# Kernel tuning notes

Hardware: AMD Instinct MI355X
Metric: run time of the kernel (lower is better)

Reference implementation:

```python
import jax, jax.numpy as jnp
import numpy as np

D_MODEL = 1024
NUM_HEADS = 16
THETA = 10000.0
B, T = 2, 2048


def _rope(x, pos, theta_base):
    # x: (b, h, t, d_h); interleaved pairs (x0,x1),(x2,x3),... per the
    # rearrange '... (c d) -> ... c d' with d=2 in the original module.
    d = x.shape[-1]
    half = d // 2
    inv_freq = 1.0 / (theta_base ** (2.0 * jnp.arange(half, dtype=jnp.float32) / d))
    ang = pos.astype(jnp.float32)[:, None] * inv_freq[None, :]  # (t, half)
    sin = jnp.sin(ang)[None, None]  # (1,1,t,half)
    cos = jnp.cos(ang)[None, None]
    x1 = x[..., 0::2]
    x2 = x[..., 1::2]
    r1 = x1 * cos - x2 * sin
    r2 = x1 * sin + x2 * cos
    return jnp.stack([r1, r2], axis=-1).reshape(x.shape)


def setup_inputs() -> dict:
    key = jax.random.key(0)
    k0, k1, k2, k3, k4 = jax.random.split(key, 5)
    sigma = (2.0 / (D_MODEL + D_MODEL)) ** 0.5
    return {
        "in_features": jax.random.normal(k0, (B, T, D_MODEL), dtype=jnp.float32),
        "Wq": jax.random.normal(k1, (D_MODEL, D_MODEL), dtype=jnp.float32) * sigma,
        "Wk": jax.random.normal(k2, (D_MODEL, D_MODEL), dtype=jnp.float32) * sigma,
        "Wv": jax.random.normal(k3, (D_MODEL, D_MODEL), dtype=jnp.float32) * sigma,
        "Wo": jax.random.normal(k4, (D_MODEL, D_MODEL), dtype=jnp.float32) * sigma,
        "token_positions": jnp.arange(T, dtype=jnp.int32),
    }


def reference(in_features, Wq, Wk, Wv, Wo, token_positions):
    b, t, d_model = in_features.shape
    h = NUM_HEADS
    d_h = d_model // h
    # Fused-style QKV projections (x @ W.T, weights stored (in, out))
    q = in_features @ Wq.T
    k = in_features @ Wk.T
    v = in_features @ Wv.T
    # (b, t, h*d_h) -> (b, h, t, d_h)
    q = q.reshape(b, t, h, d_h).transpose(0, 2, 1, 3)
    k = k.reshape(b, t, h, d_h).transpose(0, 2, 1, 3)
    v = v.reshape(b, t, h, d_h).transpose(0, 2, 1, 3)
    q = _rope(q, token_positions, THETA)
    k = _rope(k, token_positions, THETA)
    scale = 1.0 / jnp.sqrt(jnp.asarray(d_h, dtype=q.dtype))
    scores = jnp.einsum('bhqd,bhkd->bhqk', q, k) * scale
    causal = jnp.tril(jnp.ones((t, t), dtype=bool))
    scores = jnp.where(causal[None, None], scores, -jnp.inf)
    attn = jax.nn.softmax(scores, axis=-1)
    out = jnp.einsum('bhqk,bhkd->bhqd', attn, v)
    out = out.transpose(0, 2, 1, 3).reshape(b, t, h * d_h)
    return out @ Wo.T
```

## Files before the change

kernel.cpp:

```cpp
#include <hip/hip_runtime.h>

#define D_MODEL 1024
#define NUM_HEADS 16
#define DH 64
#define B_SZ 2
#define T_SZ 2048
#define M_ROWS (B_SZ * T_SZ)

typedef __bf16 bf16;
typedef __bf16 bf16x4 __attribute__((ext_vector_type(4)));
typedef __bf16 bf16x8 __attribute__((ext_vector_type(8)));
typedef float f32x4 __attribute__((ext_vector_type(4)));

__device__ __forceinline__ void async_copy16(const bf16* g, bf16* l) {
  __builtin_amdgcn_global_load_lds(
      (const __attribute__((address_space(1))) void*)g,
      (__attribute__((address_space(3))) void*)l, 16, 0, 0);
}

#define NX (M_ROWS * D_MODEL / 4)
#define NW (D_MODEL * D_MODEL / 4)

__global__ __launch_bounds__(256) void cast_all(
    const float* __restrict__ X, const float* __restrict__ Wq,
    const float* __restrict__ Wk, const float* __restrict__ Wv,
    const float* __restrict__ Wo,
    bf16* __restrict__ Xb, bf16* __restrict__ Wqb, bf16* __restrict__ Wkb,
    bf16* __restrict__ Wvb, bf16* __restrict__ Wob) {
  int i = blockIdx.x * 256 + threadIdx.x;
  const float* s; bf16* d; int off;
  if (i < NX) {
    s = X; d = Xb; off = i;
  } else {
    int j = i - NX;
    int w = j >> 18;
    off = j & (NW - 1);
    if (w == 0)      { s = Wq; d = Wqb; }
    else if (w == 1) { s = Wk; d = Wkb; }
    else if (w == 2) { s = Wv; d = Wvb; }
    else             { s = Wo; d = Wob; }
  }
  float4 v = ((const float4*)s)[off];
  bf16x4 o;
  o[0] = (bf16)v.x; o[1] = (bf16)v.y; o[2] = (bf16)v.z; o[3] = (bf16)v.w;
  ((bf16x4*)d)[off] = o;
}

#define KLN 0.28782313662425f
#define BK 32
#define NKT (D_MODEL / BK)

__global__ __launch_bounds__(512, 4) void qkv_gemm(
    const bf16* __restrict__ Xb,
    const bf16* __restrict__ Wqb, const bf16* __restrict__ Wkb,
    const bf16* __restrict__ Wvb, const int* __restrict__ pos,
    bf16* __restrict__ Q, bf16* __restrict__ K, bf16* __restrict__ VT) {
  __shared__ bf16 LA[3][128 * BK];
  __shared__ bf16 LB[3][256 * BK];

  int tid = threadIdx.x;
  int wave = tid >> 6, lane = tid & 63;
  int wm = wave >> 2, wn = wave & 3;
  int l15 = lane & 15, quad = lane >> 4;

  int row0 = blockIdx.x * 128;
  int col0 = blockIdx.y * 256;
  int sel = col0 >> 10;
  int nb = col0 & 1023;
  const bf16* W = (sel == 0) ? Wqb : (sel == 1) ? Wkb : Wvb;

  int srow = tid >> 2;
  int scol = 8 * ((tid & 3) ^ ((tid >> 3) & 3));
  const bf16* Ag = Xb + (size_t)(row0 + srow) * D_MODEL + scol;
  const bf16* Bg = W + (size_t)(nb + srow) * D_MODEL + scol;
  int ldst = tid * 8;

  int swz = 8 * (quad ^ ((l15 >> 1) & 3));
  int aoff = (wm * 64 + l15) * BK + swz;
  int boff = (wn * 64 + l15) * BK + swz;

  f32x4 acc[4][4];
#pragma unroll
  for (int mi = 0; mi < 4; ++mi)
#pragma unroll
    for (int nj = 0; nj < 4; ++nj) acc[mi][nj] = (f32x4){0.f, 0.f, 0.f, 0.f};

#define STAGE(bq, pt)                                                        \
  do {                                                                       \
    int k0_ = (pt) * BK;                                                     \
    async_copy16(Ag + k0_, &LA[bq][ldst]);                                   \
    async_copy16(Bg + k0_, &LB[bq][ldst]);                                   \
    async_copy16(Bg + k0_ + (size_t)128 * D_MODEL, &LB[bq][ldst + 4096]);    \
  } while (0)

  STAGE(0, 0);
  STAGE(1, 1);
  asm volatile("s_waitcnt vmcnt(3)" ::: "memory");
  __builtin_amdgcn_s_barrier();
  __builtin_amdgcn_sched_barrier(0);

  int cur = 0;
  for (int kt = 0; kt < NKT; ++kt) {
    const bf16* La = LA[cur];
    const bf16* Lb = LB[cur];
    bf16x8 a[4], b[4];
#pragma unroll
    for (int mi = 0; mi < 4; ++mi)
      a[mi] = *(const bf16x8*)&La[aoff + mi * 16 * BK];
#pragma unroll
    for (int nj = 0; nj < 4; ++nj)
      b[nj] = *(const bf16x8*)&Lb[boff + nj * 16 * BK];

    if (kt + 2 < NKT) {
      int nbuf = cur + 2 >= 3 ? cur - 1 : cur + 2;
      STAGE(nbuf, kt + 2);
      asm volatile("s_waitcnt vmcnt(3) lgkmcnt(0)" ::: "memory");
    } else {
      asm volatile("s_waitcnt vmcnt(0) lgkmcnt(0)" ::: "memory");
    }
    __builtin_amdgcn_s_barrier();
    __builtin_amdgcn_sched_barrier(0);

    __builtin_amdgcn_s_setprio(1);
#pragma unroll
    for (int mi = 0; mi < 4; ++mi)
#pragma unroll
      for (int nj = 0; nj < 4; ++nj)
        acc[mi][nj] = __builtin_amdgcn_mfma_f32_16x16x32_bf16(
            a[mi], b[nj], acc[mi][nj], 0, 0, 0);
    __builtin_amdgcn_s_setprio(0);

    cur = cur == 2 ? 0 : cur + 1;
  }
#undef STAGE

  if (sel == 1) {
    bool even = (l15 & 1) == 0;
#pragma unroll
    for (int nj = 0; nj < 4; ++nj) {
      float fr = __expf(-(float)((nj * 16 + (l15 & 14)) >> 1) * KLN);
#pragma unroll
      for (int mi = 0; mi < 4; ++mi)
#pragma unroll
        for (int r = 0; r < 4; ++r) {
          float p = (float)pos[(row0 + wm * 64 + mi * 16 + quad * 4 + r) &
                               (T_SZ - 1)];
          float v = acc[mi][nj][r];
          float pn = __shfl_xor(v, 1);
          float s, c;
          __sincosf(p * fr, &s, &c);
          acc[mi][nj][r] = even ? (v * c - pn * s) : (pn * s + v * c);
        }
    }
  }

  if (sel == 2) {
    int b = row0 >> 11;
    int t0 = row0 & (T_SZ - 1);
#pragma unroll
    for (int mi = 0; mi < 4; ++mi) {
      int t = t0 + wm * 64 + mi * 16 + quad * 4;
#pragma unroll
      for (int nj = 0; nj < 4; ++nj) {
        int col = nb + wn * 64 + nj * 16 + l15;
        int h = col >> 6;
        int d = col & 63;
        bf16x4 ov;
#pragma unroll
        for (int r = 0; r < 4; ++r) ov[r] = (bf16)acc[mi][nj][r];
        *(bf16x4*)&VT[((size_t)(b * NUM_HEADS + h) * DH + d) * T_SZ + t] = ov;
      }
    }
  } else {
    bf16* Out = (sel == 0) ? Q : K;
#pragma unroll
    for (int mi = 0; mi < 4; ++mi) {
      int row = row0 + wm * 64 + mi * 16 + quad * 4;
#pragma unroll
      for (int nj = 0; nj < 4; ++nj) {
        int col = nb + wn * 64 + nj * 16 + l15;
#pragma unroll
        for (int r = 0; r < 4; ++r)
          Out[(size_t)(row + r) * D_MODEL + col] = (bf16)acc[mi][nj][r];
      }
    }
  }
}

#define KST 72

__global__ __launch_bounds__(256, 3) void attn_kernel(
    const bf16* __restrict__ Q, const bf16* __restrict__ K,
    const bf16* __restrict__ VT, const int* __restrict__ pos,
    bf16* __restrict__ AO) {
  __shared__ bf16 KV[2 * 64 * KST];
  __shared__ float lred[4][4][16];
  bf16* Kt = KV;
  bf16* Vt = KV + 64 * KST;

  int bh = blockIdx.x;
  int qi = 31 - (int)blockIdx.y;
  int bb = bh >> 4, h = bh & 15;
  int tid = threadIdx.x;
  int wave = tid >> 6, lane = tid & 63;
  int l15 = lane & 15, quad = lane >> 4;
  int w16 = wave * 16;

  int q0 = qi * 64;
  size_t grow = (size_t)bb * T_SZ + q0;

  bf16x8 bq[4][2];
#pragma unroll
  for (int qt = 0; qt < 4; ++qt) {
    const bf16* Qp = Q + (grow + qt * 16 + l15) * D_MODEL + h * DH + quad * 8;
    bq[qt][0] = *(const bf16x8*)(Qp);
    bq[qt][1] = *(const bf16x8*)(Qp + 32);
    float p = (float)pos[q0 + qt * 16 + l15];
#pragma unroll
    for (int jj = 0; jj < 4; ++jj) {
      int i0 = quad * 4 + jj;
      float s, c;
      __sincosf(p * __expf(-(float)i0 * KLN), &s, &c);
      float x1 = (float)bq[qt][0][2 * jj], x2 = (float)bq[qt][0][2 * jj + 1];
      bq[qt][0][2 * jj]     = (bf16)(x1 * c - x2 * s);
      bq[qt][0][2 * jj + 1] = (bf16)(x1 * s + x2 * c);
      __sincosf(p * __expf(-(float)(i0 + 16) * KLN), &s, &c);
      float y1 = (float)bq[qt][1][2 * jj], y2 = (float)bq[qt][1][2 * jj + 1];
      bq[qt][1][2 * jj]     = (bf16)(y1 * c - y2 * s);
      bq[qt][1][2 * jj + 1] = (bf16)(y1 * s + y2 * c);
    }
  }

  f32x4 o[4][4];
#pragma unroll
  for (int dt = 0; dt < 4; ++dt)
#pragma unroll
    for (int qt = 0; qt < 4; ++qt) o[dt][qt] = (f32x4){0.f, 0.f, 0.f, 0.f};
  float l_acc[4] = {0.f, 0.f, 0.f, 0.f};

  int srow = tid >> 2;
  int sc = (tid & 3) * 16;
  const bf16* Kg = K + ((size_t)bb * T_SZ + srow) * D_MODEL + h * DH + sc;
  const bf16* Vg = VT + ((size_t)bh * DH + srow) * T_SZ + sc;
  bf16* Kl = &Kt[srow * KST + sc];
  bf16* Vl = &Vt[srow * KST + sc];

  int nchunks = qi + 1;

  bf16x8 kr0 = *(const bf16x8*)(Kg);
  bf16x8 kr1 = *(const bf16x8*)(Kg + 8);
  bf16x8 vr0 = *(const bf16x8*)(Vg);
  bf16x8 vr1 = *(const bf16x8*)(Vg + 8);

  for (int t = 0; t < nchunks; ++t) {
    __syncthreads();
    *(bf16x8*)(Kl) = kr0;
    *(bf16x8*)(Kl + 8) = kr1;
    *(bf16x8*)(Vl) = vr0;
    *(bf16x8*)(Vl + 8) = vr1;
    if (t + 1 < nchunks) {
      const bf16* Kn = Kg + (size_t)(t + 1) * 64 * D_MODEL;
      const bf16* Vn = Vg + (t + 1) * 64;
      kr0 = *(const bf16x8*)(Kn);
      kr1 = *(const bf16x8*)(Kn + 8);
      vr0 = *(const bf16x8*)(Vn);
      vr1 = *(const bf16x8*)(Vn + 8);
    }
    __syncthreads();

    bf16x8 ak0 = *(const bf16x8*)&Kt[(w16 + l15) * KST + quad * 8];
    bf16x8 ak1 = *(const bf16x8*)&Kt[(w16 + l15) * KST + 32 + quad * 8];
    f32x4 st[4];
#pragma unroll
    for (int qt = 0; qt < 4; ++qt) {
      f32x4 s4 = (f32x4){0.f, 0.f, 0.f, 0.f};
      s4 = __builtin_amdgcn_mfma_f32_16x16x32_bf16(ak0, bq[qt][0], s4, 0, 0, 0);
      s4 = __builtin_amdgcn_mfma_f32_16x16x32_bf16(ak1, bq[qt][1], s4, 0, 0, 0);
      st[qt] = s4;
    }

    bool last = (t == nchunks - 1);
    bf16x4 pb[4];
#pragma unroll
    for (int qt = 0; qt < 4; ++qt) {
      float ps = 0.f;
#pragma unroll
      for (int j = 0; j < 4; ++j) {
        float p = __expf(st[qt][j] * 0.125f);
        if (last) {
          int cl = w16 + quad * 4 + j;
          p = (cl > qt * 16 + l15) ? 0.f : p;
        }
        pb[qt][j] = (bf16)p;
        ps += p;
      }
      l_acc[qt] += ps;
    }

#pragma unroll
    for (int dt = 0; dt < 4; ++dt) {
      bf16x4 vb = *(const bf16x4*)&Vt[(dt * 16 + l15) * KST + w16 + quad * 4];
#pragma unroll
      for (int qt = 0; qt < 4; ++qt)
        asm("v_mfma_f32_16x16x16_bf16 %0, %1, %2, %0"
            : "+v"(o[dt][qt])
            : "v"(pb[qt]), "v"(vb));
    }
  }

#pragma unroll
  for (int qt = 0; qt < 4; ++qt) {
    l_acc[qt] += __shfl_xor(l_acc[qt], 16);
    l_acc[qt] += __shfl_xor(l_acc[qt], 32);
  }
  if (lane < 16) {
#pragma unroll
    for (int qt = 0; qt < 4; ++qt) lred[wave][qt][lane] = l_acc[qt];
  }

  __syncthreads();
  float* red = (float*)KV;

#pragma unroll
  for (int s = 1; s <= 3; ++s) {
#pragma unroll
    for (int qt = 0; qt < 4; ++qt)
      if (((qt - s) & 3) == wave) {
#pragma unroll
        for (int dt = 0; dt < 4; ++dt)
          *(f32x4*)&red[qt * 1024 + dt * 256 + lane * 4] = o[dt][qt];
      }
    __syncthreads();
#pragma unroll
    for (int qt = 0; qt < 4; ++qt)
      if (qt == wave) {
#pragma unroll
        for (int dt = 0; dt < 4; ++dt)
          o[dt][qt] += *(const f32x4*)&red[qt * 1024 + dt * 256 + lane * 4];
      }
    __syncthreads();
  }

#pragma unroll
  for (int qt = 0; qt < 4; ++qt)
    if (qt == wave) {
      float inv[4];
#pragma unroll
      for (int r = 0; r < 4; ++r) {
        int qq = quad * 4 + r;
        float ls = lred[0][qt][qq] + lred[1][qt][qq] + lred[2][qt][qq] +
                   lred[3][qt][qq];
        inv[r] = 1.0f / ls;
      }
#pragma unroll
      for (int dt = 0; dt < 4; ++dt)
#pragma unroll
        for (int r = 0; r < 4; ++r)
          AO[(grow + qt * 16 + quad * 4 + r) * D_MODEL + h * DH + dt * 16 +
             l15] = (bf16)(o[dt][qt][r] * inv[r]);
    }
}

__global__ __launch_bounds__(256) void out_gemm(
    const bf16* __restrict__ AO, const bf16* __restrict__ Wob,
    float* __restrict__ out) {
  __shared__ bf16 As[128 * 32];
  __shared__ bf16 Bs[64 * 32];

  int tid = threadIdx.x;
  int wave = tid >> 6, lane = tid & 63;
  int l15 = lane & 15, quad = lane >> 4;

  int row0 = blockIdx.x * 128;
  int nb = blockIdx.y * 64;

  int srow = tid >> 2;
  int schunk = tid & 3;
  const bf16* Ag = AO + (size_t)(row0 + srow) * D_MODEL + schunk * 8;
  const bf16* Bg = Wob + (size_t)(nb + srow) * D_MODEL + schunk * 8;
  bf16* Al0 = &As[srow * 32 + schunk * 8];
  bf16* Al1 = &As[(srow + 64) * 32 + schunk * 8];
  bf16* Bl = &Bs[srow * 32 + schunk * 8];

  f32x4 acc[2][4];
#pragma unroll
  for (int i = 0; i < 2; ++i)
#pragma unroll
    for (int j = 0; j < 4; ++j) acc[i][j] = (f32x4){0.f, 0.f, 0.f, 0.f};

  for (int k0 = 0; k0 < D_MODEL; k0 += 32) {
    async_copy16(Ag + k0, Al0);
    async_copy16(Ag + k0 + (size_t)64 * D_MODEL, Al1);
    async_copy16(Bg + k0, Bl);
    __syncthreads();

    bf16x8 af[2], bfr[4];
#pragma unroll
    for (int i = 0; i < 2; ++i)
      af[i] = *(const bf16x8*)&As[(wave * 32 + i * 16 + l15) * 32 + quad * 8];
#pragma unroll
    for (int j = 0; j < 4; ++j)
      bfr[j] = *(const bf16x8*)&Bs[(j * 16 + l15) * 32 + quad * 8];
#pragma unroll
    for (int i = 0; i < 2; ++i)
#pragma unroll
      for (int j = 0; j < 4; ++j)
        acc[i][j] = __builtin_amdgcn_mfma_f32_16x16x32_bf16(af[i], bfr[j],
                                                            acc[i][j], 0, 0, 0);
    __syncthreads();
  }

#pragma unroll
  for (int i = 0; i < 2; ++i) {
    int row = row0 + wave * 32 + i * 16 + quad * 4;
#pragma unroll
    for (int j = 0; j < 4; ++j) {
      int col = nb + j * 16 + l15;
#pragma unroll
      for (int r = 0; r < 4; ++r)
        out[(size_t)(row + r) * D_MODEL + col] = acc[i][j][r];
    }
  }
}

extern "C" void kernel_launch(void* const* d_in, const int* in_sizes, int n_in,
                              void* d_out, int out_size, void* d_ws, size_t ws_size,
                              hipStream_t stream) {
  const float* X  = (const float*)d_in[0];
  const float* Wq = (const float*)d_in[1];
  const float* Wk = (const float*)d_in[2];
  const float* Wv = (const float*)d_in[3];
  const float* Wo = (const float*)d_in[4];
  const int*  pos = (const int*)d_in[5];
  float* out = (float*)d_out;

  char* w = (char*)d_ws;
  bf16* Xb  = (bf16*)w;  w += (size_t)M_ROWS * D_MODEL * 2;
  bf16* Wqb = (bf16*)w;  w += (size_t)D_MODEL * D_MODEL * 2;
  bf16* Wkb = (bf16*)w;  w += (size_t)D_MODEL * D_MODEL * 2;
  bf16* Wvb = (bf16*)w;  w += (size_t)D_MODEL * D_MODEL * 2;
  bf16* Wob = (bf16*)w;  w += (size_t)D_MODEL * D_MODEL * 2;
  bf16* Qb  = (bf16*)w;  w += (size_t)M_ROWS * D_MODEL * 2;
  bf16* Kb  = (bf16*)w;  w += (size_t)M_ROWS * D_MODEL * 2;
  bf16* VT  = (bf16*)w;  w += (size_t)M_ROWS * D_MODEL * 2;
  bf16* AO  = (bf16*)w;  w += (size_t)M_ROWS * D_MODEL * 2;

  cast_all<<<(NX + 4 * NW) / 256, 256, 0, stream>>>(X, Wq, Wk, Wv, Wo,
                                                    Xb, Wqb, Wkb, Wvb, Wob);
  qkv_gemm<<<dim3(M_ROWS / 128, 3 * D_MODEL / 256), 512, 0, stream>>>(
      Xb, Wqb, Wkb, Wvb, pos, Qb, Kb, VT);
  attn_kernel<<<dim3(B_SZ * NUM_HEADS, T_SZ / 64), 256, 0, stream>>>(
      Qb, Kb, VT, pos, AO);
  out_gemm<<<dim3(M_ROWS / 128, D_MODEL / 64), 256, 0, stream>>>(AO, Wob, out);
}
```

Before: 173.0 us.

## Load K and V fragments directly from global memory instead of staging through LDS

The attention kernel no longer copies each 64-key K/V chunk into shared memory behind two barriers. Each wave only ever uses its own 16 keys, so it now loads its K MFMA operands and V fragments straight from global memory into registers. The next chunk's K is prefetched after the QK MFMAs, and V is loaded at the top of each iteration so the softmax work can hide its latency. This drops the per-chunk __syncthreads and the LDS round trip. In exchange, global accesses are less coalesced, V arrives in 8-byte pieces, and all load latency now depends on cache behaviour. The reduction scratch becomes its own shared buffer.

```diff
diff --git a/kernel.cpp b/kernel.cpp
--- a/kernel.cpp
+++ b/kernel.cpp
@@ -187,16 +187,12 @@
   }
 }
 
-#define KST 72
-
 __global__ __launch_bounds__(256, 3) void attn_kernel(
     const bf16* __restrict__ Q, const bf16* __restrict__ K,
     const bf16* __restrict__ VT, const int* __restrict__ pos,
     bf16* __restrict__ AO) {
-  __shared__ bf16 KV[2 * 64 * KST];
+  __shared__ float red[4096];
   __shared__ float lred[4][4][16];
-  bf16* Kt = KV;
-  bf16* Vt = KV + 64 * KST;
 
   int bh = blockIdx.x;
   int qi = 31 - (int)blockIdx.y;
@@ -238,38 +234,22 @@
     for (int qt = 0; qt < 4; ++qt) o[dt][qt] = (f32x4){0.f, 0.f, 0.f, 0.f};
   float l_acc[4] = {0.f, 0.f, 0.f, 0.f};
 
-  int srow = tid >> 2;
-  int sc = (tid & 3) * 16;
-  const bf16* Kg = K + ((size_t)bb * T_SZ + srow) * D_MODEL + h * DH + sc;
-  const bf16* Vg = VT + ((size_t)bh * DH + srow) * T_SZ + sc;
-  bf16* Kl = &Kt[srow * KST + sc];
-  bf16* Vl = &Vt[srow * KST + sc];
-
   int nchunks = qi + 1;
 
-  bf16x8 kr0 = *(const bf16x8*)(Kg);
-  bf16x8 kr1 = *(const bf16x8*)(Kg + 8);
-  bf16x8 vr0 = *(const bf16x8*)(Vg);
-  bf16x8 vr1 = *(const bf16x8*)(Vg + 8);
+  const bf16* kp =
+      K + ((size_t)bb * T_SZ + w16 + l15) * D_MODEL + h * DH + quad * 8;
+  const bf16* vp = VT + ((size_t)bh * DH + l15) * T_SZ + w16 + quad * 4;
+
+  bf16x8 ak0 = *(const bf16x8*)(kp);
+  bf16x8 ak1 = *(const bf16x8*)(kp + 32);
 
   for (int t = 0; t < nchunks; ++t) {
-    __syncthreads();
-    *(bf16x8*)(Kl) = kr0;
-    *(bf16x8*)(Kl + 8) = kr1;
-    *(bf16x8*)(Vl) = vr0;
-    *(bf16x8*)(Vl + 8) = vr1;
-    if (t + 1 < nchunks) {
-      const bf16* Kn = Kg + (size_t)(t + 1) * 64 * D_MODEL;
-      const bf16* Vn = Vg + (t + 1) * 64;
-      kr0 = *(const bf16x8*)(Kn);
-      kr1 = *(const bf16x8*)(Kn + 8);
-      vr0 = *(const bf16x8*)(Vn);
-      vr1 = *(const bf16x8*)(Vn + 8);
-    }
-    __syncthreads();
-
-    bf16x8 ak0 = *(const bf16x8*)&Kt[(w16 + l15) * KST + quad * 8];
-    bf16x8 ak1 = *(const bf16x8*)&Kt[(w16 + l15) * KST + 32 + quad * 8];
+    bf16x4 vb[4];
+    const bf16* vpt = vp + t * 64;
+#pragma unroll
+    for (int dt = 0; dt < 4; ++dt)
+      vb[dt] = *(const bf16x4*)(vpt + (size_t)dt * 16 * T_SZ);
+
     f32x4 st[4];
 #pragma unroll
     for (int qt = 0; qt < 4; ++qt) {
@@ -277,6 +257,12 @@
       s4 = __builtin_amdgcn_mfma_f32_16x16x32_bf16(ak0, bq[qt][0], s4, 0, 0, 0);
       s4 = __builtin_amdgcn_mfma_f32_16x16x32_bf16(ak1, bq[qt][1], s4, 0, 0, 0);
       st[qt] = s4;
+    }
+
+    if (t + 1 < nchunks) {
+      const bf16* kn = kp + (size_t)(t + 1) * 64 * D_MODEL;
+      ak0 = *(const bf16x8*)(kn);
+      ak1 = *(const bf16x8*)(kn + 32);
     }
 
     bool last = (t == nchunks - 1);
@@ -298,14 +284,12 @@
     }
 
 #pragma unroll
-    for (int dt = 0; dt < 4; ++dt) {
-      bf16x4 vb = *(const bf16x4*)&Vt[(dt * 16 + l15) * KST + w16 + quad * 4];
+    for (int dt = 0; dt < 4; ++dt)
 #pragma unroll
       for (int qt = 0; qt < 4; ++qt)
         asm("v_mfma_f32_16x16x16_bf16 %0, %1, %2, %0"
             : "+v"(o[dt][qt])
-            : "v"(pb[qt]), "v"(vb));
-    }
+            : "v"(pb[qt]), "v"(vb[dt]));
   }
 
 #pragma unroll
@@ -317,9 +301,6 @@
 #pragma unroll
     for (int qt = 0; qt < 4; ++qt) lred[wave][qt][lane] = l_acc[qt];
   }
-
-  __syncthreads();
-  float* red = (float*)KV;
 
 #pragma unroll
   for (int s = 1; s <= 3; ++s) {
```

Result: slower. 191.3 us (+10.5%).

## Fuse fp32-to-bf16 casts into QKV and output GEMM loaders, drop cast kernel

Applied to the files above, without the earlier changes.

Removes the separate cast kernel and has the QKV GEMM and output GEMM read fp32 inputs and weights directly. The values are converted to bf16 in registers before being written to LDS. The QKV GEMM moves from a 3-stage async global-to-LDS pipeline to a 2-stage register-staged double buffer. This saves a launch and a full read-write pass over X and the weights. In exchange, the GEMMs read twice as many bytes per tile and repeat the weight conversion in every block, and the pipelining is shallower with extra VALU conversion work.

```diff
diff --git a/kernel.cpp b/kernel.cpp
--- a/kernel.cpp
+++ b/kernel.cpp
@@ -18,45 +18,17 @@
       (__attribute__((address_space(3))) void*)l, 16, 0, 0);
 }
 
-#define NX (M_ROWS * D_MODEL / 4)
-#define NW (D_MODEL * D_MODEL / 4)
-
-__global__ __launch_bounds__(256) void cast_all(
-    const float* __restrict__ X, const float* __restrict__ Wq,
-    const float* __restrict__ Wk, const float* __restrict__ Wv,
-    const float* __restrict__ Wo,
-    bf16* __restrict__ Xb, bf16* __restrict__ Wqb, bf16* __restrict__ Wkb,
-    bf16* __restrict__ Wvb, bf16* __restrict__ Wob) {
-  int i = blockIdx.x * 256 + threadIdx.x;
-  const float* s; bf16* d; int off;
-  if (i < NX) {
-    s = X; d = Xb; off = i;
-  } else {
-    int j = i - NX;
-    int w = j >> 18;
-    off = j & (NW - 1);
-    if (w == 0)      { s = Wq; d = Wqb; }
-    else if (w == 1) { s = Wk; d = Wkb; }
-    else if (w == 2) { s = Wv; d = Wvb; }
-    else             { s = Wo; d = Wob; }
-  }
-  float4 v = ((const float4*)s)[off];
-  bf16x4 o;
-  o[0] = (bf16)v.x; o[1] = (bf16)v.y; o[2] = (bf16)v.z; o[3] = (bf16)v.w;
-  ((bf16x4*)d)[off] = o;
-}
-
 #define KLN 0.28782313662425f
 #define BK 32
 #define NKT (D_MODEL / BK)
 
 __global__ __launch_bounds__(512, 4) void qkv_gemm(
-    const bf16* __restrict__ Xb,
-    const bf16* __restrict__ Wqb, const bf16* __restrict__ Wkb,
-    const bf16* __restrict__ Wvb, const int* __restrict__ pos,
+    const float* __restrict__ X,
+    const float* __restrict__ Wq, const float* __restrict__ Wk,
+    const float* __restrict__ Wv, const int* __restrict__ pos,
     bf16* __restrict__ Q, bf16* __restrict__ K, bf16* __restrict__ VT) {
-  __shared__ bf16 LA[3][128 * BK];
-  __shared__ bf16 LB[3][256 * BK];
+  __shared__ bf16 LA[2][128 * BK];
+  __shared__ bf16 LB[2][256 * BK];
 
   int tid = threadIdx.x;
   int wave = tid >> 6, lane = tid & 63;
@@ -67,13 +39,13 @@
   int col0 = blockIdx.y * 256;
   int sel = col0 >> 10;
   int nb = col0 & 1023;
-  const bf16* W = (sel == 0) ? Wqb : (sel == 1) ? Wkb : Wvb;
+  const float* W = (sel == 0) ? Wq : (sel == 1) ? Wk : Wv;
 
   int srow = tid >> 2;
-  int scol = 8 * ((tid & 3) ^ ((tid >> 3) & 3));
-  const bf16* Ag = Xb + (size_t)(row0 + srow) * D_MODEL + scol;
-  const bf16* Bg = W + (size_t)(nb + srow) * D_MODEL + scol;
-  int ldst = tid * 8;
+  int chnk = tid & 3;
+  const float* Ag = X + (size_t)(row0 + srow) * D_MODEL + chnk * 8;
+  const float* Bg = W + (size_t)(nb + srow) * D_MODEL + chnk * 8;
+  int woff = srow * BK + 8 * (chnk ^ ((srow >> 1) & 3));
 
   int swz = 8 * (quad ^ ((l15 >> 1) & 3));
   int aoff = (wm * 64 + l15) * BK + swz;
@@ -85,24 +57,44 @@
 #pragma unroll
     for (int nj = 0; nj < 4; ++nj) acc[mi][nj] = (f32x4){0.f, 0.f, 0.f, 0.f};
 
-#define STAGE(bq, pt)                                                        \
+  f32x4 ra0, ra1, rb0, rb1, rb2, rb3;
+
+#define LOADR(pt)                                                            \
   do {                                                                       \
-    int k0_ = (pt) * BK;                                                     \
-    async_copy16(Ag + k0_, &LA[bq][ldst]);                                   \
-    async_copy16(Bg + k0_, &LB[bq][ldst]);                                   \
-    async_copy16(Bg + k0_ + (size_t)128 * D_MODEL, &LB[bq][ldst + 4096]);    \
+    const float* Ap = Ag + (size_t)(pt)*BK;                                  \
+    const float* Bp = Bg + (size_t)(pt)*BK;                                  \
+    ra0 = *(const f32x4*)(Ap);                                               \
+    ra1 = *(const f32x4*)(Ap + 4);                                           \
+    rb0 = *(const f32x4*)(Bp);                                               \
+    rb1 = *(const f32x4*)(Bp + 4);                                           \
+    rb2 = *(const f32x4*)(Bp + (size_t)128 * D_MODEL);                       \
+    rb3 = *(const f32x4*)(Bp + (size_t)128 * D_MODEL + 4);                   \
   } while (0)
 
-  STAGE(0, 0);
-  STAGE(1, 1);
-  asm volatile("s_waitcnt vmcnt(3)" ::: "memory");
+#define WRITEL(bq)                                                           \
+  do {                                                                       \
+    bf16x8 va, vb0, vb1;                                                     \
+    _Pragma("unroll") for (int j = 0; j < 4; ++j) {                          \
+      va[j] = (bf16)ra0[j];   va[j + 4] = (bf16)ra1[j];                      \
+      vb0[j] = (bf16)rb0[j];  vb0[j + 4] = (bf16)rb1[j];                     \
+      vb1[j] = (bf16)rb2[j];  vb1[j + 4] = (bf16)rb3[j];                     \
+    }                                                                        \
+    *(bf16x8*)&LA[bq][woff] = va;                                            \
+    *(bf16x8*)&LB[bq][woff] = vb0;                                           \
+    *(bf16x8*)&LB[bq][woff + 4096] = vb1;                                    \
+  } while (0)
+
+  LOADR(0);
+  asm volatile("s_waitcnt vmcnt(0)" ::: "memory");
+  WRITEL(0);
+  LOADR(1);
+  asm volatile("s_waitcnt lgkmcnt(0)" ::: "memory");
   __builtin_amdgcn_s_barrier();
   __builtin_amdgcn_sched_barrier(0);
 
-  int cur = 0;
   for (int kt = 0; kt < NKT; ++kt) {
-    const bf16* La = LA[cur];
-    const bf16* Lb = LB[cur];
+    const bf16* La = LA[kt & 1];
+    const bf16* Lb = LB[kt & 1];
     bf16x8 a[4], b[4];
 #pragma unroll
     for (int mi = 0; mi < 4; ++mi)
@@ -111,13 +103,12 @@
     for (int nj = 0; nj < 4; ++nj)
       b[nj] = *(const bf16x8*)&Lb[boff + nj * 16 * BK];
 
-    if (kt + 2 < NKT) {
-      int nbuf = cur + 2 >= 3 ? cur - 1 : cur + 2;
-      STAGE(nbuf, kt + 2);
-      asm volatile("s_waitcnt vmcnt(3) lgkmcnt(0)" ::: "memory");
-    } else {
-      asm volatile("s_waitcnt vmcnt(0) lgkmcnt(0)" ::: "memory");
-    }
+    if (kt + 1 < NKT) {
+      asm volatile("s_waitcnt vmcnt(0)" ::: "memory");
+      WRITEL((kt + 1) & 1);
+      if (kt + 2 < NKT) LOADR(kt + 2);
+    }
+    asm volatile("s_waitcnt lgkmcnt(0)" ::: "memory");
     __builtin_amdgcn_s_barrier();
     __builtin_amdgcn_sched_barrier(0);
 
@@ -129,10 +120,9 @@
         acc[mi][nj] = __builtin_amdgcn_mfma_f32_16x16x32_bf16(
             a[mi], b[nj], acc[mi][nj], 0, 0, 0);
     __builtin_amdgcn_s_setprio(0);
-
-    cur = cur == 2 ? 0 : cur + 1;
-  }
-#undef STAGE
+  }
+#undef LOADR
+#undef WRITEL
 
   if (sel == 1) {
     bool even = (l15 & 1) == 0;
@@ -362,7 +352,7 @@
 }
 
 __global__ __launch_bounds__(256) void out_gemm(
-    const bf16* __restrict__ AO, const bf16* __restrict__ Wob,
+    const bf16* __restrict__ AO, const float* __restrict__ Wo,
     float* __restrict__ out) {
   __shared__ bf16 As[128 * 32];
   __shared__ bf16 Bs[64 * 32];
@@ -377,10 +367,11 @@
   int srow = tid >> 2;
   int schunk = tid & 3;
   const bf16* Ag = AO + (size_t)(row0 + srow) * D_MODEL + schunk * 8;
-  const bf16* Bg = Wob + (size_t)(nb + srow) * D_MODEL + schunk * 8;
+  const float* Bg = Wo + (size_t)(nb + (srow & 63)) * D_MODEL + schunk * 8;
   bf16* Al0 = &As[srow * 32 + schunk * 8];
   bf16* Al1 = &As[(srow + 64) * 32 + schunk * 8];
-  bf16* Bl = &Bs[srow * 32 + schunk * 8];
+  bf16* Bl = &Bs[(srow & 63) * 32 + schunk * 8];
+  bool bstage = srow < 64;
 
   f32x4 acc[2][4];
 #pragma unroll
@@ -391,9 +382,18 @@
   for (int k0 = 0; k0 < D_MODEL; k0 += 32) {
     async_copy16(Ag + k0, Al0);
     async_copy16(Ag + k0 + (size_t)64 * D_MODEL, Al1);
-    async_copy16(Bg + k0, Bl);
-    __syncthreads();
-
+    {
+      f32x4 w0 = *(const f32x4*)(Bg + k0);
+      f32x4 w1 = *(const f32x4*)(Bg + k0 + 4);
+      bf16x8 wb;
+#pragma unroll
+      for (int j = 0; j < 4; ++j) {
+        wb[j] = (bf16)w0[j];
+        wb[j + 4] = (bf16)w1[j];
+      }
+      *(bf16x8*)Bl = wb;
+    }
+    __syncthreads();
     bf16x8 af[2], bfr[4];
 #pragma unroll
     for (int i = 0; i < 2; ++i)
@@ -409,6 +409,7 @@
                                                             acc[i][j], 0, 0, 0);
     __syncthreads();
   }
+  (void)bstage;
 
 #pragma unroll
   for (int i = 0; i < 2; ++i) {
@@ -435,21 +436,14 @@
   float* out = (float*)d_out;
 
   char* w = (char*)d_ws;
-  bf16* Xb  = (bf16*)w;  w += (size_t)M_ROWS * D_MODEL * 2;
-  bf16* Wqb = (bf16*)w;  w += (size_t)D_MODEL * D_MODEL * 2;
-  bf16* Wkb = (bf16*)w;  w += (size_t)D_MODEL * D_MODEL * 2;
-  bf16* Wvb = (bf16*)w;  w += (size_t)D_MODEL * D_MODEL * 2;
-  bf16* Wob = (bf16*)w;  w += (size_t)D_MODEL * D_MODEL * 2;
   bf16* Qb  = (bf16*)w;  w += (size_t)M_ROWS * D_MODEL * 2;
   bf16* Kb  = (bf16*)w;  w += (size_t)M_ROWS * D_MODEL * 2;
   bf16* VT  = (bf16*)w;  w += (size_t)M_ROWS * D_MODEL * 2;
   bf16* AO  = (bf16*)w;  w += (size_t)M_ROWS * D_MODEL * 2;
 
-  cast_all<<<(NX + 4 * NW) / 256, 256, 0, stream>>>(X, Wq, Wk, Wv, Wo,
-                                                    Xb, Wqb, Wkb, Wvb, Wob);
   qkv_gemm<<<dim3(M_ROWS / 128, 3 * D_MODEL / 256), 512, 0, stream>>>(
-      Xb, Wqb, Wkb, Wvb, pos, Qb, Kb, VT);
+      X, Wq, Wk, Wv, pos, Qb, Kb, VT);
   attn_kernel<<<dim3(B_SZ * NUM_HEADS, T_SZ / 64), 256, 0, stream>>>(
       Qb, Kb, VT, pos, AO);
-  out_gemm<<<dim3(M_ROWS / 128, D_MODEL / 64), 256, 0, stream>>>(AO, Wob, out);
+  out_gemm<<<dim3(M_ROWS / 128, D_MODEL / 64), 256, 0, stream>>>(AO, Wo, out);
 }
```

Result: slower. 184.7 us (+6.8%).
